# Kernel optimization log

Hardware: AMD Instinct MI355X
Metric: run time of the kernel (lower is better)

## Reference

```python
import jax, jax.numpy as jnp
import numpy as np

H, C, T = 4, 64, 6  # heads, per-head dim, num edge types


def segment_softmax(e, seg, n):
    # e: [E, H] logits, seg: [E] destination ids
    m = jax.ops.segment_max(e, seg, num_segments=n)
    m = jnp.where(jnp.isfinite(m), m, 0.0)
    w = jnp.exp(e - m[seg])
    s = jax.ops.segment_sum(w, seg, num_segments=n)
    return w / (s[seg] + 1e-16)


def gatv2(x_src, x_dst, ei, Wsrc, Wdst, att, b):
    # GATv2Conv (bipartite, add_self_loops=False, concat heads)
    n_dst = x_dst.shape[0]
    hs = (x_src @ Wsrc).reshape(x_src.shape[0], H, C)  # lin_l(x_src)
    hd = (x_dst @ Wdst).reshape(n_dst, H, C)            # lin_r(x_dst)
    src, dst = ei[0], ei[1]
    m = hs[src] + hd[dst]                                # [E,H,C]
    e = jnp.einsum('ehc,hc->eh', jax.nn.leaky_relu(m, 0.2), att)
    a = segment_softmax(e, dst, n_dst)                   # [E,H]
    out = jax.ops.segment_sum(a[:, :, None] * hs[src], dst, num_segments=n_dst)
    return out.reshape(n_dst, H * C) + b


def setup_inputs() -> dict:
    key = jax.random.key(0)
    ks = jax.random.split(key, 20)
    Npkg, N, Din, E, Dedge = 50000, 50000, 128, 200000, 8
    F = H * C  # 256
    K = T * Dedge  # num_clusters = 48 (forced by concat in subgraph_cls)
    s = 0.05
    return {
        'x_pkg': jax.random.normal(ks[0], (Npkg, Din), jnp.float32),
        'x_dst': jax.random.normal(ks[1], (T, N, Din), jnp.float32),
        'edge_attr': jax.random.uniform(ks[2], (T, E, Dedge), dtype=jnp.float32),
        'node_mask': jnp.ones((N,), jnp.float32),
        'W1_src': jax.random.normal(ks[3], (T, Din, F), jnp.float32) * s,
        'W1_dst': jax.random.normal(ks[4], (T, Din, F), jnp.float32) * s,
        'att1': jax.random.normal(ks[5], (T, H, C), jnp.float32) * s,
        'b1': jnp.zeros((T, F), jnp.float32),
        'W2_src': jax.random.normal(ks[6], (T, Din, F), jnp.float32) * s,
        'W2_dst': jax.random.normal(ks[7], (T, F, F), jnp.float32) * s,
        'att2': jax.random.normal(ks[8], (T, H, C), jnp.float32) * s,
        'b2': jnp.zeros((T, F), jnp.float32),
        'W_pool': jax.random.normal(ks[9], (F, K), jnp.float32) * s,
        'b_pool': jnp.zeros((K,), jnp.float32),
        'W_cls': jax.random.normal(ks[10], (F + 1, 1), jnp.float32) * s,
        'b_cls': jnp.zeros((1,), jnp.float32),
        'edge_index': jax.random.randint(ks[11], (T, 2, E), 0, N, dtype=jnp.int32),
        'batch': jnp.zeros((N,), jnp.int32),
    }


def reference(x_pkg, x_dst, edge_attr, node_mask, W1_src, W1_dst, att1, b1,
              W2_src, W2_dst, att2, b2, W_pool, b_pool, W_cls, b_cls,
              edge_index, batch):
    # node masking (edge_mask is all-ones -> bernoulli keeps every edge)
    xp = x_pkg * node_mask[:x_pkg.shape[0], None]
    outs = []
    for t in range(T):  # fixed set of 6 hetero edge types
        xd = x_dst[t] * node_mask[:x_dst.shape[1], None]
        h1 = jax.nn.relu(gatv2(xp, xd, edge_index[t], W1_src[t], W1_dst[t], att1[t], b1[t]))
        h2 = gatv2(xp, h1, edge_index[t], W2_src[t], W2_dst[t], att2[t], b2[t])
        outs.append(h2)
    h = outs[-1]  # forward keeps only the last node type's pooled embedding
    # DiffPool: soft assignment then pooled features
    s_assign = jax.nn.softmax(h @ W_pool + b_pool, axis=-1)  # [N, K]
    x_pooled = s_assign.T @ h                                 # [K, F]
    # global edge-attribute aggregation
    agg_edge = edge_attr.mean(axis=1).reshape(-1)             # [T*Dedge] == K
    feat = jnp.concatenate([x_pooled, agg_edge[:, None]], axis=-1)  # [K, F+1]
    return jax.nn.sigmoid(feat @ W_cls + b_cls)               # [K, 1]
```

## Files before the change

kernel.cpp:

```cpp
#include <hip/hip_runtime.h>
#include <math.h>

#define NN 50000
#define DIN 128
#define FDIM 256
#define EE 200000
#define TT 6
#define DE 8
#define KC 48
#define NB ((NN + 255)/256)

typedef __attribute__((ext_vector_type(8))) short bf16x8;
typedef __attribute__((ext_vector_type(8))) unsigned short u16x8;
typedef __attribute__((ext_vector_type(4))) float f32x4;

__device__ inline unsigned short f2b(float f){
  unsigned u = __float_as_uint(f);
  unsigned r = u + 0x7FFFu + ((u >> 16) & 1u);
  return (unsigned short)(r >> 16);
}
__device__ inline float b2f(unsigned short u){ return __uint_as_float(((unsigned)u) << 16); }

__global__ void zero_deg_agg(int* __restrict__ deg, int* __restrict__ aggE){
  int i = blockIdx.x*256 + threadIdx.x;
  if (i < NN) deg[i] = 0;
  if (i < 64) aggE[i] = 0;
}

__global__ void count_deg(const int* __restrict__ dst, int* __restrict__ deg){
  int i = blockIdx.x*256 + threadIdx.x;
  if (i < EE) atomicAdd(&deg[dst[i]], 1);
}

__global__ __launch_bounds__(256) void scan_blk(const int* __restrict__ deg, int* __restrict__ rp,
                                                int* __restrict__ bsum){
  __shared__ int sm[256];
  int i = blockIdx.x*256 + threadIdx.x;
  int v = (i < NN) ? deg[i] : 0;
  sm[threadIdx.x] = v;
  __syncthreads();
  #pragma unroll
  for (int off = 1; off < 256; off <<= 1){
    int t = (threadIdx.x >= (unsigned)off) ? sm[threadIdx.x - off] : 0;
    __syncthreads();
    sm[threadIdx.x] += t;
    __syncthreads();
  }
  if (i < NN) rp[i] = sm[threadIdx.x] - v;
  if (threadIdx.x == 255) bsum[blockIdx.x] = sm[255];
}

__global__ __launch_bounds__(256) void scan_sums(const int* __restrict__ bsum, int* __restrict__ boff){
  __shared__ int sm[256];
  int v = (threadIdx.x < NB) ? bsum[threadIdx.x] : 0;
  sm[threadIdx.x] = v;
  __syncthreads();
  #pragma unroll
  for (int off = 1; off < 256; off <<= 1){
    int t = (threadIdx.x >= (unsigned)off) ? sm[threadIdx.x - off] : 0;
    __syncthreads();
    sm[threadIdx.x] += t;
    __syncthreads();
  }
  if (threadIdx.x < NB) boff[threadIdx.x] = sm[threadIdx.x] - v;
}

__global__ __launch_bounds__(256) void scan_add(int* __restrict__ rp, const int* __restrict__ boff,
                                                int* __restrict__ cursor){
  int i = blockIdx.x*256 + threadIdx.x;
  if (i < NN){
    int r = rp[i] + boff[blockIdx.x];
    rp[i] = r;
    cursor[i] = r;
  }
  if (i == 0) rp[NN] = EE;
}

__global__ void scatter_edges(const int* __restrict__ src, const int* __restrict__ dst,
                              int* __restrict__ cursor, int* __restrict__ srt){
  int i = blockIdx.x*256 + threadIdx.x;
  if (i < EE){ int pos = atomicAdd(&cursor[dst[i]], 1); srt[pos] = src[i]; }
}

__global__ void cvt_wt_all(const float* __restrict__ W1s, const float* __restrict__ W2s,
                           const float* __restrict__ W1d, const float* __restrict__ W2d,
                           unsigned short* __restrict__ Wtall, unsigned short* __restrict__ Wt2d){
  int n = blockIdx.x;
  int which = blockIdx.y;
  if (which == 3){
    for (int k = threadIdx.x; k < FDIM; k += 256)
      Wt2d[(size_t)n*FDIM + k] = f2b(W2d[(size_t)k*256 + n]);
  } else {
    const float* W = (which == 0) ? W1s : (which == 1) ? W2s : W1d;
    unsigned short* o = Wtall + (size_t)which*256*DIN + (size_t)n*DIN;
    for (int k = threadIdx.x; k < DIN; k += 256)
      o[k] = f2b(W[(size_t)k*256 + n]);
  }
}

__global__ __launch_bounds__(256) void gemm_l1(const float* __restrict__ Apkg, const float* __restrict__ Adst,
                                               const unsigned short* __restrict__ Wtall,
                                               const float* __restrict__ mask,
                                               unsigned short* __restrict__ Chs1,
                                               unsigned short* __restrict__ Chs2,
                                               unsigned short* __restrict__ Chd1){
  __shared__ short Al[128][56];
  __shared__ short Bl[128][56];
  int tid = threadIdx.x;
  int lane = tid & 63;
  int w = tid >> 6;
  int wm = w >> 1, wn = w & 1;
  int by = blockIdx.y;
  const float* A = (by >= 4) ? Adst : Apkg;
  const unsigned short* Wt = Wtall + (size_t)(by >> 1)*256*DIN;
  unsigned short* Co = (by < 2) ? Chs1 : (by < 4) ? Chs2 : Chd1;
  int row0 = blockIdx.x * 128, col0 = (by & 1) * 128;
  int fr = lane & 15;
  int kb = lane >> 4;
  f32x4 acc[4][4];
  #pragma unroll
  for (int i = 0; i < 4; i++)
    #pragma unroll
    for (int j = 0; j < 4; j++)
      acc[i][j] = (f32x4){0.f, 0.f, 0.f, 0.f};

  for (int k0 = 0; k0 < DIN; k0 += 32){
    u16x8 ra[2]; bf16x8 rb[2];
    #pragma unroll
    for (int p = 0; p < 2; p++){
      int idx = tid + p*256;
      int r = idx >> 2, ch = idx & 3;
      int gr = row0 + r;
      u16x8 o = (u16x8){0,0,0,0,0,0,0,0};
      if (gr < NN){
        float mv = mask[gr];
        const float* ap = A + (size_t)gr*DIN + k0 + ch*8;
        float4 a0 = *(const float4*)(ap);
        float4 a1 = *(const float4*)(ap + 4);
        o[0]=f2b(a0.x*mv); o[1]=f2b(a0.y*mv); o[2]=f2b(a0.z*mv); o[3]=f2b(a0.w*mv);
        o[4]=f2b(a1.x*mv); o[5]=f2b(a1.y*mv); o[6]=f2b(a1.z*mv); o[7]=f2b(a1.w*mv);
      }
      ra[p] = o;
      rb[p] = *(const bf16x8*)(Wt + (size_t)(col0 + r)*DIN + k0 + ch*8);
    }
    __syncthreads();
    #pragma unroll
    for (int p = 0; p < 2; p++){
      int idx = tid + p*256;
      int r = idx >> 2, ch = idx & 3;
      *(u16x8*)(&Al[r][ch*8]) = ra[p];
      *(bf16x8*)(&Bl[r][ch*8]) = rb[p];
    }
    __syncthreads();
    bf16x8 af[4], bfr[4];
    #pragma unroll
    for (int i = 0; i < 4; i++) af[i]  = *(const bf16x8*)(&Al[wm*64 + i*16 + fr][kb*8]);
    #pragma unroll
    for (int j = 0; j < 4; j++) bfr[j] = *(const bf16x8*)(&Bl[wn*64 + j*16 + fr][kb*8]);
    #pragma unroll
    for (int i = 0; i < 4; i++)
      #pragma unroll
      for (int j = 0; j < 4; j++)
        acc[i][j] = __builtin_amdgcn_mfma_f32_16x16x32_bf16(af[i], bfr[j], acc[i][j], 0, 0, 0);
  }
  #pragma unroll
  for (int i = 0; i < 4; i++){
    #pragma unroll
    for (int q = 0; q < 4; q++){
      int grow = row0 + wm*64 + i*16 + kb*4 + q;
      if (grow < NN){
        #pragma unroll
        for (int j = 0; j < 4; j++)
          Co[(size_t)grow*256 + col0 + wn*64 + j*16 + fr] = f2b(acc[i][j][q]);
      }
    }
  }
}

__global__ __launch_bounds__(256) void gemm_bf16(const short* __restrict__ A, const short* __restrict__ Wt,
                                                 unsigned short* __restrict__ Cb, int M, int K){
  __shared__ short Al[128][56];
  __shared__ short Bl[128][56];
  int tid = threadIdx.x;
  int lane = tid & 63;
  int w = tid >> 6;
  int wm = w >> 1, wn = w & 1;
  int row0 = blockIdx.x * 128, col0 = blockIdx.y * 128;
  int fr = lane & 15;
  int kb = lane >> 4;
  f32x4 acc[4][4];
  #pragma unroll
  for (int i = 0; i < 4; i++)
    #pragma unroll
    for (int j = 0; j < 4; j++)
      acc[i][j] = (f32x4){0.f, 0.f, 0.f, 0.f};

  for (int k0 = 0; k0 < K; k0 += 32){
    bf16x8 ra[2], rb[2];
    #pragma unroll
    for (int p = 0; p < 2; p++){
      int idx = tid + p*256;
      int r = idx >> 2, ch = idx & 3;
      int gr = row0 + r;
      if (gr < M) ra[p] = *(const bf16x8*)(A + (size_t)gr*K + k0 + ch*8);
      else        ra[p] = (bf16x8){0,0,0,0,0,0,0,0};
      rb[p] = *(const bf16x8*)(Wt + (size_t)(col0 + r)*K + k0 + ch*8);
    }
    __syncthreads();
    #pragma unroll
    for (int p = 0; p < 2; p++){
      int idx = tid + p*256;
      int r = idx >> 2, ch = idx & 3;
      *(bf16x8*)(&Al[r][ch*8]) = ra[p];
      *(bf16x8*)(&Bl[r][ch*8]) = rb[p];
    }
    __syncthreads();
    bf16x8 af[4], bfr[4];
    #pragma unroll
    for (int i = 0; i < 4; i++) af[i]  = *(const bf16x8*)(&Al[wm*64 + i*16 + fr][kb*8]);
    #pragma unroll
    for (int j = 0; j < 4; j++) bfr[j] = *(const bf16x8*)(&Bl[wn*64 + j*16 + fr][kb*8]);
    #pragma unroll
    for (int i = 0; i < 4; i++)
      #pragma unroll
      for (int j = 0; j < 4; j++)
        acc[i][j] = __builtin_amdgcn_mfma_f32_16x16x32_bf16(af[i], bfr[j], acc[i][j], 0, 0, 0);
  }
  #pragma unroll
  for (int i = 0; i < 4; i++){
    #pragma unroll
    for (int q = 0; q < 4; q++){
      int grow = row0 + wm*64 + i*16 + kb*4 + q;
      if (grow < M){
        #pragma unroll
        for (int j = 0; j < 4; j++)
          Cb[(size_t)grow*256 + col0 + wn*64 + j*16 + fr] = f2b(acc[i][j][q]);
      }
    }
  }
}

__global__ __launch_bounds__(256) void gat_fused(const int* __restrict__ rp, const int* __restrict__ srt,
                                                 const unsigned short* __restrict__ hs,
                                                 const unsigned short* __restrict__ hd,
                                                 const float* __restrict__ att, const float* __restrict__ bias,
                                                 unsigned short* __restrict__ outb, int do_relu){
  int n = blockIdx.x*4 + (threadIdx.x >> 6);
  int lane = threadIdx.x & 63;
  if (n >= NN) return;
  const float4 av = *(const float4*)(att + lane*4);
  ushort4 ud = *(const ushort4*)(hd + (size_t)n*256 + lane*4);
  float d0 = b2f(ud.x), d1 = b2f(ud.y), d2 = b2f(ud.z), d3 = b2f(ud.w);
  int beg = rp[n], end = rp[n+1];
  float4 acc = {0.f,0.f,0.f,0.f};
  float sw = 0.f;
  for (int i = beg; i < end; i++){
    int s = srt[i];
    ushort4 uh = *(const ushort4*)(hs + (size_t)s*256 + lane*4);
    float h0 = b2f(uh.x), h1 = b2f(uh.y), h2 = b2f(uh.z), h3 = b2f(uh.w);
    float m0 = h0 + d0, m1 = h1 + d1, m2 = h2 + d2, m3 = h3 + d3;
    m0 = (m0 > 0.f) ? m0 : 0.2f*m0;
    m1 = (m1 > 0.f) ? m1 : 0.2f*m1;
    m2 = (m2 > 0.f) ? m2 : 0.2f*m2;
    m3 = (m3 > 0.f) ? m3 : 0.2f*m3;
    float p = m0*av.x + m1*av.y + m2*av.z + m3*av.w;
    #pragma unroll
    for (int msk = 8; msk > 0; msk >>= 1) p += __shfl_xor(p, msk);
    float w = expf(fminf(p, 80.f));
    acc.x = fmaf(w, h0, acc.x);
    acc.y = fmaf(w, h1, acc.y);
    acc.z = fmaf(w, h2, acc.z);
    acc.w = fmaf(w, h3, acc.w);
    sw += w;
  }
  float inv = 1.f / (sw + 1e-16f);
  const float4 b4 = *(const float4*)(bias + lane*4);
  float4 r;
  r.x = acc.x*inv + b4.x;
  r.y = acc.y*inv + b4.y;
  r.z = acc.z*inv + b4.z;
  r.w = acc.w*inv + b4.w;
  if (do_relu){
    r.x = fmaxf(r.x, 0.f); r.y = fmaxf(r.y, 0.f);
    r.z = fmaxf(r.z, 0.f); r.w = fmaxf(r.w, 0.f);
  }
  ushort4 o;
  o.x = f2b(r.x); o.y = f2b(r.y); o.z = f2b(r.z); o.w = f2b(r.w);
  *(ushort4*)(outb + (size_t)n*256 + lane*4) = o;
}

__global__ __launch_bounds__(256) void pool_logits_mfma(const unsigned short* __restrict__ h2b,
                                                        const float* __restrict__ Wp,
                                                        const float* __restrict__ bp,
                                                        unsigned short* __restrict__ sass,
                                                        float* __restrict__ xp){
  __shared__ short Al[128][56];
  __shared__ short Bn[KC][264];
  int tid = threadIdx.x;
  int lane = tid & 63;
  int w = tid >> 6;
  int row0 = blockIdx.x * 128;
  int fr = lane & 15;
  int kb = lane >> 4;
  if (blockIdx.x == 0){
    for (int i = tid; i < KC*FDIM; i += 256) xp[i] = 0.f;
  }
  for (int idx = tid; idx < 256*KC; idx += 256){
    int k = idx / KC, n = idx % KC;
    Bn[n][k] = f2b(Wp[idx]);
  }
  f32x4 acc[2][3];
  #pragma unroll
  for (int i = 0; i < 2; i++)
    #pragma unroll
    for (int j = 0; j < 3; j++)
      acc[i][j] = (f32x4){0.f, 0.f, 0.f, 0.f};

  for (int k0 = 0; k0 < 256; k0 += 32){
    bf16x8 ra[2];
    #pragma unroll
    for (int p = 0; p < 2; p++){
      int idx = tid + p*256;
      int r = idx >> 2, ch = idx & 3;
      int gr = row0 + r;
      if (gr < NN) ra[p] = *(const bf16x8*)((const short*)h2b + (size_t)gr*256 + k0 + ch*8);
      else         ra[p] = (bf16x8){0,0,0,0,0,0,0,0};
    }
    __syncthreads();
    #pragma unroll
    for (int p = 0; p < 2; p++){
      int idx = tid + p*256;
      int r = idx >> 2, ch = idx & 3;
      *(bf16x8*)(&Al[r][ch*8]) = ra[p];
    }
    __syncthreads();
    bf16x8 af[2], bfr[3];
    #pragma unroll
    for (int i = 0; i < 2; i++) af[i]  = *(const bf16x8*)(&Al[w*32 + i*16 + fr][kb*8]);
    #pragma unroll
    for (int j = 0; j < 3; j++) bfr[j] = *(const bf16x8*)(&Bn[j*16 + fr][k0 + kb*8]);
    #pragma unroll
    for (int i = 0; i < 2; i++)
      #pragma unroll
      for (int j = 0; j < 3; j++)
        acc[i][j] = __builtin_amdgcn_mfma_f32_16x16x32_bf16(af[i], bfr[j], acc[i][j], 0, 0, 0);
  }
  float bb[3];
  #pragma unroll
  for (int j = 0; j < 3; j++) bb[j] = bp[j*16 + fr];
  #pragma unroll
  for (int i = 0; i < 2; i++){
    #pragma unroll
    for (int q = 0; q < 4; q++){
      int grow = row0 + w*32 + i*16 + kb*4 + q;
      float v0 = acc[i][0][q] + bb[0];
      float v1 = acc[i][1][q] + bb[1];
      float v2 = acc[i][2][q] + bb[2];
      float m = fmaxf(v0, fmaxf(v1, v2));
      #pragma unroll
      for (int msk = 8; msk > 0; msk >>= 1) m = fmaxf(m, __shfl_xor(m, msk));
      float e0 = expf(v0 - m), e1 = expf(v1 - m), e2 = expf(v2 - m);
      float s = e0 + e1 + e2;
      #pragma unroll
      for (int msk = 8; msk > 0; msk >>= 1) s += __shfl_xor(s, msk);
      float inv = 1.f / s;
      if (grow < NN){
        unsigned short* so = sass + (size_t)grow*KC;
        so[fr]      = f2b(e0 * inv);
        so[16 + fr] = f2b(e1 * inv);
        so[32 + fr] = f2b(e2 * inv);
      }
    }
  }
}

#define PCH 64
#define NPART ((NN + PCH - 1)/PCH)
__global__ __launch_bounds__(256) void pooled_partial(const unsigned short* __restrict__ sass,
                                                      const unsigned short* __restrict__ h2b,
                                                      float* __restrict__ part){
  __shared__ float sld[PCH][KC];
  int t = threadIdx.x;
  int base = blockIdx.x * PCH;
  int cnt = min(PCH, NN - base);
  for (int idx = t; idx < cnt*KC; idx += 256)
    sld[idx/KC][idx%KC] = b2f(sass[(size_t)(base + idx/KC)*KC + idx%KC]);
  __syncthreads();
  float acc[KC];
  #pragma unroll
  for (int k = 0; k < KC; k++) acc[k] = 0.f;
  for (int n = 0; n < cnt; n++){
    float v = b2f(h2b[(size_t)(base + n)*256 + t]);
    #pragma unroll
    for (int k = 0; k < KC; k++) acc[k] = fmaf(sld[n][k], v, acc[k]);
  }
  float* po = part + (size_t)blockIdx.x*KC*256;
  #pragma unroll
  for (int k = 0; k < KC; k++) po[k*256 + t] = acc[k];
}

#define PSPL 8
__global__ __launch_bounds__(256) void pooled_reduce(const float* __restrict__ part, float* __restrict__ xp){
  int idx = blockIdx.x*256 + threadIdx.x;
  const int per = (NPART + PSPL - 1)/PSPL;
  int p0 = blockIdx.y * per;
  int p1 = min(p0 + per, NPART);
  float s0 = 0.f, s1 = 0.f;
  int p = p0;
  for (; p + 1 < p1; p += 2){
    s0 += part[(size_t)p*KC*256 + idx];
    s1 += part[(size_t)(p+1)*KC*256 + idx];
  }
  if (p < p1) s0 += part[(size_t)p*KC*256 + idx];
  atomicAdd(&xp[idx], s0 + s1);
}

#define BPT 128
__global__ __launch_bounds__(256) void edge_attr_mean(const float* __restrict__ ea, float* __restrict__ out){
  int t   = blockIdx.x / BPT;
  int blk = blockIdx.x % BPT;
  const int NF4 = EE * 2;
  const int per_blk = (NF4 + BPT - 1) / BPT;
  int i0 = blk * per_blk;
  int i1 = min(i0 + per_blk, NF4);
  const float4* base = (const float4*)(ea + (size_t)t*EE*DE);
  float s[8] = {0,0,0,0,0,0,0,0};
  for (int i = i0 + (int)threadIdx.x; i < i1; i += 256){
    float4 v = base[i];
    int db = (i & 1) * 4;
    s[db+0] += v.x; s[db+1] += v.y; s[db+2] += v.z; s[db+3] += v.w;
  }
  __shared__ float red[256];
  for (int d = 0; d < 8; d++){
    red[threadIdx.x] = s[d];
    __syncthreads();
    for (int off = 128; off > 0; off >>= 1){
      if (threadIdx.x < (unsigned)off) red[threadIdx.x] += red[threadIdx.x + off];
      __syncthreads();
    }
    if (threadIdx.x == 0) atomicAdd(&out[t*DE + d], red[0] / (float)EE);
    __syncthreads();
  }
}

__global__ void final_cls(const float* __restrict__ xp, const float* __restrict__ agg,
                          const float* __restrict__ Wc, const float* __restrict__ bc,
                          float* __restrict__ out){
  int k = threadIdx.x;
  if (k < KC){
    float s = bc[0];
    for (int f = 0; f < 256; f++) s = fmaf(xp[k*256 + f], Wc[f], s);
    s = fmaf(agg[k], Wc[256], s);
    out[k] = 1.f/(1.f + expf(-s));
  }
}

extern "C" void kernel_launch(void* const* d_in, const int* in_sizes, int n_in,
                              void* d_out, int out_size, void* d_ws, size_t ws_size,
                              hipStream_t stream) {
  const float* x_pkg     = (const float*)d_in[0];
  const float* x_dst     = (const float*)d_in[1];
  const float* edge_attr = (const float*)d_in[2];
  const float* node_mask = (const float*)d_in[3];
  const float* W1_src    = (const float*)d_in[4];
  const float* W1_dst    = (const float*)d_in[5];
  const float* att1      = (const float*)d_in[6];
  const float* b1        = (const float*)d_in[7];
  const float* W2_src    = (const float*)d_in[8];
  const float* W2_dst    = (const float*)d_in[9];
  const float* att2      = (const float*)d_in[10];
  const float* b2        = (const float*)d_in[11];
  const float* W_pool    = (const float*)d_in[12];
  const float* b_pool    = (const float*)d_in[13];
  const float* W_cls     = (const float*)d_in[14];
  const float* b_cls     = (const float*)d_in[15];
  const int*   edge_index= (const int*)d_in[16];
  float* out = (float*)d_out;

  const int T5 = TT - 1;
  const float* W1s5 = W1_src + (size_t)T5*DIN*FDIM;
  const float* W1d5 = W1_dst + (size_t)T5*DIN*FDIM;
  const float* a1_5 = att1   + (size_t)T5*FDIM;
  const float* b1_5 = b1     + (size_t)T5*FDIM;
  const float* W2s5 = W2_src + (size_t)T5*DIN*FDIM;
  const float* W2d5 = W2_dst + (size_t)T5*FDIM*FDIM;
  const float* a2_5 = att2   + (size_t)T5*FDIM;
  const float* b2_5 = b2     + (size_t)T5*FDIM;
  const float* xd5  = x_dst  + (size_t)T5*NN*DIN;
  const int* src5   = edge_index + (size_t)T5*2*EE;
  const int* dst5   = src5 + EE;

  float* buf0 = (float*)d_ws;
  float* buf1 = buf0 + (size_t)NN*FDIM;
  float* buf2 = buf1 + (size_t)NN*FDIM;
  float* xpool= buf2 + (size_t)NN*FDIM;
  float* aggE = xpool + KC*FDIM;
  int* deg    = (int*)(aggE + 64);
  int* rp     = deg + NN;
  int* cursor = rp + NN + 1;
  int* srt    = cursor + NN;
  unsigned short* Wtall = (unsigned short*)(srt + EE);
  unsigned short* Wt2d  = Wtall + (size_t)3*256*DIN;
  int* bsum = (int*)(Wt2d + (size_t)256*FDIM);
  int* boff = bsum + NB;
  unsigned short* hs1b = (unsigned short*)buf0;
  unsigned short* hs2b = hs1b + (size_t)NN*FDIM;
  unsigned short* hd1b = (unsigned short*)buf1;
  unsigned short* h1b  = hd1b + (size_t)NN*FDIM;
  unsigned short* h2b  = (unsigned short*)buf1;
  unsigned short* hd2b = (unsigned short*)buf2;
  unsigned short* sass = (unsigned short*)buf2;

  zero_deg_agg<<<(NN+255)/256, 256, 0, stream>>>(deg, (int*)aggE);
  count_deg<<<(EE+255)/256, 256, 0, stream>>>(dst5, deg);
  scan_blk<<<NB, 256, 0, stream>>>(deg, rp, bsum);
  scan_sums<<<1, 256, 0, stream>>>(bsum, boff);
  scan_add<<<NB, 256, 0, stream>>>(rp, boff, cursor);
  scatter_edges<<<(EE+255)/256, 256, 0, stream>>>(src5, dst5, cursor, srt);

  edge_attr_mean<<<TT*BPT, 256, 0, stream>>>(edge_attr, aggE);

  cvt_wt_all<<<dim3(256, 4), 256, 0, stream>>>(W1s5, W2s5, W1d5, W2d5, Wtall, Wt2d);

  gemm_l1<<<dim3((NN + 127)/128, 6), 256, 0, stream>>>(x_pkg, xd5, Wtall, node_mask,
                                                        hs1b, hs2b, hd1b);
  gat_fused<<<NN/4, 256, 0, stream>>>(rp, srt, hs1b, hd1b, a1_5, b1_5, h1b, 1);

  gemm_bf16<<<dim3((NN + 127)/128, 2), 256, 0, stream>>>((const short*)h1b, (const short*)Wt2d,
                                                          hd2b, NN, FDIM);
  gat_fused<<<NN/4, 256, 0, stream>>>(rp, srt, hs2b, hd2b, a2_5, b2_5, h2b, 0);

  pool_logits_mfma<<<(NN + 127)/128, 256, 0, stream>>>(h2b, W_pool, b_pool, sass, xpool);
  pooled_partial<<<NPART, 256, 0, stream>>>(sass, h2b, buf0);
  pooled_reduce<<<dim3(KC, PSPL), 256, 0, stream>>>(buf0, xpool);
  final_cls<<<1, 64, 0, stream>>>(xpool, aggE, W_cls, b_cls, out);
}
```

Measured before the change: 315.7 us.

## Load A tile once per block in layer-1 GEMM, unroll GAT edge loop by two

```diff
diff --git a/kernel.cpp b/kernel.cpp
--- a/kernel.cpp
+++ b/kernel.cpp
@@ -104,74 +104,82 @@
                                                unsigned short* __restrict__ Chs1,
                                                unsigned short* __restrict__ Chs2,
                                                unsigned short* __restrict__ Chd1){
-  __shared__ short Al[128][56];
+  __shared__ short Afull[128][136];
   __shared__ short Bl[128][56];
   int tid = threadIdx.x;
   int lane = tid & 63;
   int w = tid >> 6;
   int wm = w >> 1, wn = w & 1;
-  int by = blockIdx.y;
-  const float* A = (by >= 4) ? Adst : Apkg;
-  const unsigned short* Wt = Wtall + (size_t)(by >> 1)*256*DIN;
-  unsigned short* Co = (by < 2) ? Chs1 : (by < 4) ? Chs2 : Chd1;
-  int row0 = blockIdx.x * 128, col0 = (by & 1) * 128;
+  int row0 = blockIdx.x * 128;
   int fr = lane & 15;
   int kb = lane >> 4;
-  f32x4 acc[4][4];
-  #pragma unroll
-  for (int i = 0; i < 4; i++)
-    #pragma unroll
-    for (int j = 0; j < 4; j++)
-      acc[i][j] = (f32x4){0.f, 0.f, 0.f, 0.f};
-
-  for (int k0 = 0; k0 < DIN; k0 += 32){
-    u16x8 ra[2]; bf16x8 rb[2];
-    #pragma unroll
-    for (int p = 0; p < 2; p++){
-      int idx = tid + p*256;
-      int r = idx >> 2, ch = idx & 3;
-      int gr = row0 + r;
-      u16x8 o = (u16x8){0,0,0,0,0,0,0,0};
-      if (gr < NN){
-        float mv = mask[gr];
-        const float* ap = A + (size_t)gr*DIN + k0 + ch*8;
-        float4 a0 = *(const float4*)(ap);
-        float4 a1 = *(const float4*)(ap + 4);
-        o[0]=f2b(a0.x*mv); o[1]=f2b(a0.y*mv); o[2]=f2b(a0.z*mv); o[3]=f2b(a0.w*mv);
-        o[4]=f2b(a1.x*mv); o[5]=f2b(a1.y*mv); o[6]=f2b(a1.z*mv); o[7]=f2b(a1.w*mv);
+  const float* A = blockIdx.y ? Adst : Apkg;
+  #pragma unroll
+  for (int p = 0; p < 8; p++){
+    int idx = tid + p*256;
+    int r = idx >> 4, ch = idx & 15;
+    int gr = row0 + r;
+    u16x8 o = (u16x8){0,0,0,0,0,0,0,0};
+    if (gr < NN){
+      float mv = mask[gr];
+      const float* ap = A + (size_t)gr*DIN + ch*8;
+      float4 a0 = *(const float4*)(ap);
+      float4 a1 = *(const float4*)(ap + 4);
+      o[0]=f2b(a0.x*mv); o[1]=f2b(a0.y*mv); o[2]=f2b(a0.z*mv); o[3]=f2b(a0.w*mv);
+      o[4]=f2b(a1.x*mv); o[5]=f2b(a1.y*mv); o[6]=f2b(a1.z*mv); o[7]=f2b(a1.w*mv);
+    }
+    *(u16x8*)(&Afull[r][ch*8]) = o;
+  }
+  int ntile = blockIdx.y ? 2 : 4;
+  #pragma unroll 1
+  for (int t = 0; t < ntile; t++){
+    int wsel = blockIdx.y ? 2 : (t >> 1);
+    const unsigned short* Wt = Wtall + (size_t)wsel*256*DIN;
+    unsigned short* Co = blockIdx.y ? Chd1 : ((t >> 1) ? Chs2 : Chs1);
+    int col0 = (t & 1) * 128;
+    f32x4 acc[4][4];
+    #pragma unroll
+    for (int i = 0; i < 4; i++)
+      #pragma unroll
+      for (int j = 0; j < 4; j++)
+        acc[i][j] = (f32x4){0.f, 0.f, 0.f, 0.f};
+    for (int k0 = 0; k0 < DIN; k0 += 32){
+      bf16x8 rb[2];
+      #pragma unroll
+      for (int p = 0; p < 2; p++){
+        int idx = tid + p*256;
+        int r = idx >> 2, ch = idx & 3;
+        rb[p] = *(const bf16x8*)(Wt + (size_t)(col0 + r)*DIN + k0 + ch*8);
       }
-      ra[p] = o;
-      rb[p] = *(const bf16x8*)(Wt + (size_t)(col0 + r)*DIN + k0 + ch*8);
-    }
-    __syncthreads();
-    #pragma unroll
-    for (int p = 0; p < 2; p++){
-      int idx = tid + p*256;
-      int r = idx >> 2, ch = idx & 3;
-      *(u16x8*)(&Al[r][ch*8]) = ra[p];
-      *(bf16x8*)(&Bl[r][ch*8]) = rb[p];
-    }
-    __syncthreads();
-    bf16x8 af[4], bfr[4];
-    #pragma unroll
-    for (int i = 0; i < 4; i++) af[i]  = *(const bf16x8*)(&Al[wm*64 + i*16 + fr][kb*8]);
-    #pragma unroll
-    for (int j = 0; j < 4; j++) bfr[j] = *(const bf16x8*)(&Bl[wn*64 + j*16 + fr][kb*8]);
-    #pragma unroll
-    for (int i = 0; i < 4; i++)
-      #pragma unroll
-      for (int j = 0; j < 4; j++)
-        acc[i][j] = __builtin_amdgcn_mfma_f32_16x16x32_bf16(af[i], bfr[j], acc[i][j], 0, 0, 0);
-  }
-  #pragma unroll
-  for (int i = 0; i < 4; i++){
-    #pragma unroll
-    for (int q = 0; q < 4; q++){
-      int grow = row0 + wm*64 + i*16 + kb*4 + q;
-      if (grow < NN){
+      __syncthreads();
+      #pragma unroll
+      for (int p = 0; p < 2; p++){
+        int idx = tid + p*256;
+        int r = idx >> 2, ch = idx & 3;
+        *(bf16x8*)(&Bl[r][ch*8]) = rb[p];
+      }
+      __syncthreads();
+      bf16x8 af[4], bfr[4];
+      #pragma unroll
+      for (int i = 0; i < 4; i++) af[i]  = *(const bf16x8*)(&Afull[wm*64 + i*16 + fr][k0 + kb*8]);
+      #pragma unroll
+      for (int j = 0; j < 4; j++) bfr[j] = *(const bf16x8*)(&Bl[wn*64 + j*16 + fr][kb*8]);
+      #pragma unroll
+      for (int i = 0; i < 4; i++)
         #pragma unroll
         for (int j = 0; j < 4; j++)
-          Co[(size_t)grow*256 + col0 + wn*64 + j*16 + fr] = f2b(acc[i][j][q]);
+          acc[i][j] = __builtin_amdgcn_mfma_f32_16x16x32_bf16(af[i], bfr[j], acc[i][j], 0, 0, 0);
+    }
+    #pragma unroll
+    for (int i = 0; i < 4; i++){
+      #pragma unroll
+      for (int q = 0; q < 4; q++){
+        int grow = row0 + wm*64 + i*16 + kb*4 + q;
+        if (grow < NN){
+          #pragma unroll
+          for (int j = 0; j < 4; j++)
+            Co[(size_t)grow*256 + col0 + wn*64 + j*16 + fr] = f2b(acc[i][j][q]);
+        }
       }
     }
   }
@@ -254,7 +262,35 @@
   int beg = rp[n], end = rp[n+1];
   float4 acc = {0.f,0.f,0.f,0.f};
   float sw = 0.f;
-  for (int i = beg; i < end; i++){
+  int i = beg;
+  for (; i + 1 < end; i += 2){
+    int sA = srt[i], sB = srt[i+1];
+    ushort4 uA = *(const ushort4*)(hs + (size_t)sA*256 + lane*4);
+    ushort4 uB = *(const ushort4*)(hs + (size_t)sB*256 + lane*4);
+    float hA0 = b2f(uA.x), hA1 = b2f(uA.y), hA2 = b2f(uA.z), hA3 = b2f(uA.w);
+    float hB0 = b2f(uB.x), hB1 = b2f(uB.y), hB2 = b2f(uB.z), hB3 = b2f(uB.w);
+    float mA0 = hA0 + d0, mA1 = hA1 + d1, mA2 = hA2 + d2, mA3 = hA3 + d3;
+    float mB0 = hB0 + d0, mB1 = hB1 + d1, mB2 = hB2 + d2, mB3 = hB3 + d3;
+    mA0 = (mA0 > 0.f) ? mA0 : 0.2f*mA0;  mB0 = (mB0 > 0.f) ? mB0 : 0.2f*mB0;
+    mA1 = (mA1 > 0.f) ? mA1 : 0.2f*mA1;  mB1 = (mB1 > 0.f) ? mB1 : 0.2f*mB1;
+    mA2 = (mA2 > 0.f) ? mA2 : 0.2f*mA2;  mB2 = (mB2 > 0.f) ? mB2 : 0.2f*mB2;
+    mA3 = (mA3 > 0.f) ? mA3 : 0.2f*mA3;  mB3 = (mB3 > 0.f) ? mB3 : 0.2f*mB3;
+    float pA = mA0*av.x + mA1*av.y + mA2*av.z + mA3*av.w;
+    float pB = mB0*av.x + mB1*av.y + mB2*av.z + mB3*av.w;
+    #pragma unroll
+    for (int msk = 8; msk > 0; msk >>= 1){
+      pA += __shfl_xor(pA, msk);
+      pB += __shfl_xor(pB, msk);
+    }
+    float wA = expf(fminf(pA, 80.f));
+    float wB = expf(fminf(pB, 80.f));
+    acc.x = fmaf(wA, hA0, fmaf(wB, hB0, acc.x));
+    acc.y = fmaf(wA, hA1, fmaf(wB, hB1, acc.y));
+    acc.z = fmaf(wA, hA2, fmaf(wB, hB2, acc.z));
+    acc.w = fmaf(wA, hA3, fmaf(wB, hB3, acc.w));
+    sw += wA + wB;
+  }
+  if (i < end){
     int s = srt[i];
     ushort4 uh = *(const ushort4*)(hs + (size_t)s*256 + lane*4);
     float h0 = b2f(uh.x), h1 = b2f(uh.y), h2 = b2f(uh.z), h3 = b2f(uh.w);
@@ -266,12 +302,12 @@
     float p = m0*av.x + m1*av.y + m2*av.z + m3*av.w;
     #pragma unroll
     for (int msk = 8; msk > 0; msk >>= 1) p += __shfl_xor(p, msk);
-    float w = expf(fminf(p, 80.f));
-    acc.x = fmaf(w, h0, acc.x);
-    acc.y = fmaf(w, h1, acc.y);
-    acc.z = fmaf(w, h2, acc.z);
-    acc.w = fmaf(w, h3, acc.w);
-    sw += w;
+    float wv = expf(fminf(p, 80.f));
+    acc.x = fmaf(wv, h0, acc.x);
+    acc.y = fmaf(wv, h1, acc.y);
+    acc.z = fmaf(wv, h2, acc.z);
+    acc.w = fmaf(wv, h3, acc.w);
+    sw += wv;
   }
   float inv = 1.f / (sw + 1e-16f);
   const float4 b4 = *(const float4*)(bias + lane*4);
@@ -522,7 +558,7 @@
 
   cvt_wt_all<<<dim3(256, 4), 256, 0, stream>>>(W1s5, W2s5, W1d5, W2d5, Wtall, Wt2d);
 
-  gemm_l1<<<dim3((NN + 127)/128, 6), 256, 0, stream>>>(x_pkg, xd5, Wtall, node_mask,
+  gemm_l1<<<dim3((NN + 127)/128, 2), 256, 0, stream>>>(x_pkg, xd5, Wtall, node_mask,
                                                         hs1b, hs2b, hd1b);
   gat_fused<<<NN/4, 256, 0, stream>>>(rp, srt, hs1b, hd1b, a1_5, b1_5, h1b, 1);
 
```

New measurement: 283.0 us. 1.12x faster.
